# Kernel tuning notes

Hardware: AMD Instinct MI355X
Metric: run time of the kernel (lower is better)

The kernel has to match this reference:

```python
import jax, jax.numpy as jnp
import numpy as np

EPS = 1e-10


def setup_inputs() -> dict:
    key = jax.random.key(0)
    k1, k2, k3 = jax.random.split(key, 3)
    B, T, N = 32, 512, 128
    transition = jax.random.uniform(k1, (N, N), dtype=jnp.float32)
    log_emission = jax.random.normal(k2, (B, T, N), dtype=jnp.float32)
    prior = jax.random.uniform(k3, (N,), dtype=jnp.float32)
    return {"transition": transition, "log_emission": log_emission, "prior": prior}


def reference(transition, log_emission, prior):
    B, T, N = log_emission.shape
    # clamp + row-normalize transition (matches torch: clamp, clamp/sum(dim=1))
    trans = jnp.clip(transition, EPS)
    trans = jnp.clip(trans, EPS) / jnp.sum(trans, axis=1, keepdims=True)
    log_trans_T = jnp.log(trans).T  # (N, N): [next, prev]

    pr = jnp.clip(prior, EPS)
    pr = pr / jnp.sum(pr)
    log_prior = jnp.log(pr)

    # initial trellis row
    log0 = log_prior[None, :] + log_emission[:, 0]  # (B, N)
    em_rest = jnp.transpose(log_emission[:, 1:], (1, 0, 2))  # (T-1, B, N)

    def fwd_step(prev_log, em_t):
        # scores[b, next, prev] = prev_log[b, prev] + log_trans_T[next, prev]
        scores = prev_log[:, None, :] + log_trans_T[None, :, :]  # (B, N, N)
        m = jnp.max(scores, axis=-1, keepdims=True)
        e = jnp.exp(scores - m)
        Z = jnp.sum(e, axis=-1, keepdims=True)
        soft_max = jnp.squeeze(jnp.log(Z) + m, -1)  # logsumexp, (B, N)
        new_log = em_t + soft_max
        bp = e / Z  # soft backpointers, (B, N, N)
        return new_log, bp

    last_log, bps = jax.lax.scan(fwd_step, log0, em_rest)  # bps: (T-1, B, N, N)

    final_probs = jax.nn.softmax(last_log, axis=1)  # (B, N)

    def bwd_step(p_next, bp_t):
        # soft_path[t] = soft_path[t+1] @ bp[t]
        p = jnp.einsum("bn,bnm->bm", p_next, bp_t)
        return p, p

    _, path_prefix = jax.lax.scan(bwd_step, final_probs, bps, reverse=True)  # (T-1, B, N)

    soft_path = jnp.concatenate([path_prefix, final_probs[None]], axis=0)  # (T, B, N)
    return jnp.transpose(soft_path, (1, 0, 2))  # (B, T, N)
```

## Files before the change

### kernel.cpp

```cpp
#include <hip/hip_runtime.h>
#include <math.h>


#define TT 512
#define BB 32
#define NN 128
#define EPSC 1e-10f
#define TINY 1e-33f

typedef float v2f __attribute__((ext_vector_type(2)));

#define BAR() asm volatile("s_waitcnt lgkmcnt(0)\n\ts_barrier" ::: "memory")

__device__ __forceinline__ float rcp_fast(float x) {
  return __builtin_amdgcn_rcpf(x);
}

__device__ __forceinline__ float qswap1(float x) {
  return __int_as_float(__builtin_amdgcn_mov_dpp(__float_as_int(x), 0xB1, 0xF, 0xF, true));
}
__device__ __forceinline__ float qswap2(float x) {
  return __int_as_float(__builtin_amdgcn_mov_dpp(__float_as_int(x), 0x4E, 0xF, 0xF, true));
}

__device__ __forceinline__ float dotpk16(const v2f* av, const v2f tm[16]) {
  v2f a0 = av[0] * tm[0];
  v2f a1 = av[1] * tm[1];
  v2f a2 = av[2] * tm[2];
  v2f a3 = av[3] * tm[3];
  #pragma unroll
  for (int j = 4; j < 16; j += 4) {
    a0 = __builtin_elementwise_fma(av[j+0], tm[j+0], a0);
    a1 = __builtin_elementwise_fma(av[j+1], tm[j+1], a1);
    a2 = __builtin_elementwise_fma(av[j+2], tm[j+2], a2);
    a3 = __builtin_elementwise_fma(av[j+3], tm[j+3], a3);
  }
  v2f s = (a0 + a1) + (a2 + a3);
  return s.x + s.y;
}

__global__ __launch_bounds__(256, 1)
void soft_viterbi_kernel(const float* __restrict__ trans,
                         const float* __restrict__ emis,
                         const float* __restrict__ prior,
                         float* __restrict__ out) {
  const int b    = blockIdx.x;
  const int tid  = threadIdx.x;
  const int w    = tid >> 6;
  const int lane = tid & 63;
  const int k    = lane & 3;
  const int pid  = lane >> 2;
  const int n0   = 32 * w + 2 * pid;

  __shared__ __align__(16) float ubuf[2][NN];
  __shared__ __align__(16) float sarr[TT];
  __shared__ __align__(16) float red[NN];

  const float* emB = emis + (size_t)b * TT * NN;
  float* outb      = out  + (size_t)b * TT * NN;

  float2 pr2 = *(const float2*)(prior + n0);
  float2 em0 = *(const float2*)(emB + n0);
  float2 e1  = *(const float2*)(emB + 1 * NN + n0);
  float2 e2  = *(const float2*)(emB + 2 * NN + n0);
  float2 e3  = *(const float2*)(emB + 3 * NN + n0);
  float2 e4  = *(const float2*)(emB + 4 * NN + n0);
  float2 e5  = *(const float2*)(emB + 5 * NN + n0);
  pr2.x = fmaxf(pr2.x, EPSC); pr2.y = fmaxf(pr2.y, EPSC);

  if (tid < NN) {
    const float4* row = (const float4*)(trans + tid * NN);
    float s = 0.f;
    #pragma unroll 8
    for (int j = 0; j < NN / 4; ++j) {
      float4 v = row[j];
      s += fmaxf(v.x, EPSC) + fmaxf(v.y, EPSC) + fmaxf(v.z, EPSC) + fmaxf(v.w, EPSC);
    }
    red[tid] = s;
  }
  __syncthreads();

  v2f tf2[2][16];
  #pragma unroll
  for (int i = 0; i < 8; ++i) {
    #pragma unroll
    for (int c = 0; c < 4; ++c) {
      const int p = 4 * (k + 4 * i) + c;
      const float2 tv = *(const float2*)(trans + p * NN + n0);
      const float rp = red[p];
      tf2[0][2*i + (c >> 1)][c & 1] = fmaxf(tv.x, EPSC) / rp;
      tf2[1][2*i + (c >> 1)][c & 1] = fmaxf(tv.y, EPSC) / rp;
    }
  }
  v2f tb2[2][16];
  #pragma unroll
  for (int s = 0; s < 2; ++s) {
    const float inv = 1.0f / red[n0 + s];
    const float4* rr = (const float4*)(trans + (n0 + s) * NN);
    #pragma unroll
    for (int i = 0; i < 8; ++i) {
      const float4 tv = rr[k + 4 * i];
      tb2[s][2*i+0][0] = fmaxf(tv.x, EPSC) * inv;
      tb2[s][2*i+0][1] = fmaxf(tv.y, EPSC) * inv;
      tb2[s][2*i+1][0] = fmaxf(tv.z, EPSC) * inv;
      tb2[s][2*i+1][1] = fmaxf(tv.w, EPSC) * inv;
    }
  }

  float vv = (k == 0) ? (pr2.x + pr2.y) : 0.f;
  #pragma unroll
  for (int m = 1; m < 64; m <<= 1) vv += __shfl_xor(vv, m, 64);
  __syncthreads();
  if (lane == 0) red[w] = vv;
  __syncthreads();
  const float psum = (red[0] + red[1]) + (red[2] + red[3]);

  float an0 = (pr2.x / psum) * __expf(em0.x);
  float an1 = (pr2.y / psum) * __expf(em0.y);
  if (k == 0) {
    float2 a2v = make_float2(an0, an1);
    *(float2*)&ubuf[0][n0] = a2v;
    *(float2*)(outb + n0) = a2v;
  }
  float dc0 = __expf(e1.x), dc1 = __expf(e1.y);
  float2 rg0 = e4, rg1 = e5, rg2 = e2, rg3 = e3;
  BAR();

  auto fstep = [&](const float* rb, float* wb, int t, float2& slot) {
    const float r0 = rb[0];
    const float4* rb4 = (const float4*)rb;
    float4 a4[8];
    #pragma unroll
    for (int i = 0; i < 8; ++i) a4[i] = rb4[k + 4 * i];
    const v2f* av = (const v2f*)a4;
    float z0 = dotpk16(av, tf2[0]);
    float z1 = dotpk16(av, tf2[1]);
    z0 += qswap1(z0); z0 += qswap2(z0);
    z1 += qswap1(z1); z1 += qswap2(z1);
    const float rinv = rcp_fast(r0);
    an0 = (dc0 * rinv) * z0;
    an1 = (dc1 * rinv) * z1;
    dc0 = __expf(slot.x); dc1 = __expf(slot.y);
    const int tpre = (t + 5 < TT) ? (t + 5) : (TT - 1);
    const float* erow = emB + (size_t)tpre * NN;
    slot = *(const float2*)(erow + n0);
    if (k == 0) {
      float2 a2v = make_float2(an0, an1);
      *(float2*)(wb + n0) = a2v;
      if (t < TT - 1) {
        float* orow = outb + (size_t)t * NN;
        *(float2*)(orow + n0) = a2v;
      }
    }
    if (tid == 0) sarr[t - 1] = rinv;
    BAR();
  };

  fstep(ubuf[0], ubuf[1], 1, rg2);
  fstep(ubuf[1], ubuf[0], 2, rg3);
  fstep(ubuf[0], ubuf[1], 3, rg0);
  for (int t = 4; t < TT; t += 4) {
    fstep(ubuf[1], ubuf[0], t + 0, rg1);
    fstep(ubuf[0], ubuf[1], t + 1, rg2);
    fstep(ubuf[1], ubuf[0], t + 2, rg3);
    fstep(ubuf[0], ubuf[1], t + 3, rg0);
  }
  const float dl0 = dc0, dl1 = dc1;

  float v2 = (k == 0) ? (an0 + an1) : 0.f;
  #pragma unroll
  for (int m = 1; m < 64; m <<= 1) v2 += __shfl_xor(v2, m, 64);
  if (lane == 0) red[w] = v2;
  __syncthreads();
  const float total = (red[0] + red[1]) + (red[2] + red[3]);
  const float itot = 1.0f / total;
  float pc0 = an0 * itot, pc1 = an1 * itot;
  if (k == 0) *(float2*)(outb + (size_t)(TT - 1) * NN + n0) = make_float2(pc0, pc1);

  asm volatile("s_waitcnt vmcnt(0)" ::: "memory");

  float2 eb2 = *(const float2*)(emB  + (size_t)510 * NN + n0);
  float2 eb1 = *(const float2*)(emB  + (size_t)509 * NN + n0);
  float2 eb0 = *(const float2*)(emB  + (size_t)508 * NN + n0);
  float2 eb3 = *(const float2*)(emB  + (size_t)507 * NN + n0);
  float2 ac2 = *(const float2*)(outb + (size_t)510 * NN + n0);
  float2 ac1 = *(const float2*)(outb + (size_t)509 * NN + n0);
  float2 ac0 = *(const float2*)(outb + (size_t)508 * NN + n0);
  float2 ac3 = *(const float2*)(outb + (size_t)507 * NN + n0);
  const float sl = sarr[TT - 2];
  float g0 = dl0 * sl * rcp_fast(fmaxf(an0, TINY));
  float g1 = dl1 * sl * rcp_fast(fmaxf(an1, TINY));

  auto bstep = [&](float* xb, int t, float2& em_s, float2& ec_s) {
    if (k == 0) *(float2*)(xb + n0) = make_float2(pc0 * g0, pc1 * g1);
    const float sr = sarr[(t > 0) ? (t - 1) : 0];
    const float at0 = ec_s.x, at1 = ec_s.y;
    const float gn0 = __expf(em_s.x) * sr * rcp_fast(fmaxf(at0, TINY));
    const float gn1 = __expf(em_s.y) * sr * rcp_fast(fmaxf(at1, TINY));
    const int tp4 = (t >= 4) ? (t - 4) : 0;
    const float* erow = emB  + (size_t)tp4 * NN;
    const float* arow = outb + (size_t)tp4 * NN;
    em_s = *(const float2*)(erow + n0);
    ec_s = *(const float2*)(arow + n0);
    BAR();
    const float4* qb4 = (const float4*)xb;
    float4 a4[8];
    #pragma unroll
    for (int i = 0; i < 8; ++i) a4[i] = qb4[k + 4 * i];
    const v2f* av = (const v2f*)a4;
    float z0 = dotpk16(av, tb2[0]);
    float z1 = dotpk16(av, tb2[1]);
    z0 += qswap1(z0); z0 += qswap2(z0);
    z1 += qswap1(z1); z1 += qswap2(z1);
    pc0 = at0 * z0;
    pc1 = at1 * z1;
    if (k == 0) {
      float* orow = outb + (size_t)t * NN;
      *(float2*)(orow + n0) = make_float2(pc0, pc1);
    }
    g0 = gn0; g1 = gn1;
  };

  bstep(ubuf[0], 510, eb2, ac2);
  bstep(ubuf[1], 509, eb1, ac1);
  bstep(ubuf[0], 508, eb0, ac0);
  for (int t = 507; t >= 3; t -= 4) {
    bstep(ubuf[1], t - 0, eb3, ac3);
    bstep(ubuf[0], t - 1, eb2, ac2);
    bstep(ubuf[1], t - 2, eb1, ac1);
    bstep(ubuf[0], t - 3, eb0, ac0);
  }
}

extern "C" void kernel_launch(void* const* d_in, const int* in_sizes, int n_in,
                              void* d_out, int out_size, void* d_ws, size_t ws_size,
                              hipStream_t stream) {
  (void)in_sizes; (void)n_in; (void)d_ws; (void)ws_size; (void)out_size;
  const float* trans = (const float*)d_in[0];
  const float* emis  = (const float*)d_in[1];
  const float* prior = (const float*)d_in[2];
  float* out = (float*)d_out;
  soft_viterbi_kernel<<<dim3(BB), dim3(256), 0, stream>>>(trans, emis, prior, out);
}
```

Baseline: 399.4 us.

## Pack two batch sequences per 512-thread workgroup sharing barriers

Each workgroup now processes two batch elements using two 256-thread groups, with per-group LDS buffers, scale arrays and reduction slots, and launches half as many blocks. The intent is to interleave two independent serial recurrences on one CU so that one hides the other's latency. In exchange, every step's barrier now synchronises eight waves across both sequences, only half as many CUs are used, and launch_bounds(512,2) shrinks the per-thread register budget. That budget is tight for the large transition-matrix register arrays and may cause spilling.

```diff
diff --git a/kernel.cpp b/kernel.cpp
--- a/kernel.cpp
+++ b/kernel.cpp
@@ -15,7 +15,6 @@
 __device__ __forceinline__ float rcp_fast(float x) {
   return __builtin_amdgcn_rcpf(x);
 }
-
 __device__ __forceinline__ float qswap1(float x) {
   return __int_as_float(__builtin_amdgcn_mov_dpp(__float_as_int(x), 0xB1, 0xF, 0xF, true));
 }
@@ -39,22 +38,25 @@
   return s.x + s.y;
 }
 
-__global__ __launch_bounds__(256, 1)
+__global__ __launch_bounds__(512, 2)
 void soft_viterbi_kernel(const float* __restrict__ trans,
                          const float* __restrict__ emis,
                          const float* __restrict__ prior,
                          float* __restrict__ out) {
-  const int b    = blockIdx.x;
   const int tid  = threadIdx.x;
-  const int w    = tid >> 6;
+  const int GR   = tid >> 8;
+  const int t8   = tid & 255;
+  const int w    = t8 >> 6;
   const int lane = tid & 63;
   const int k    = lane & 3;
   const int pid  = lane >> 2;
   const int n0   = 32 * w + 2 * pid;
-
-  __shared__ __align__(16) float ubuf[2][NN];
-  __shared__ __align__(16) float sarr[TT];
+  const int b    = 2 * blockIdx.x + GR;
+
+  __shared__ __align__(16) float ubuf[2][2][NN];
+  __shared__ __align__(16) float sarr[2][TT];
   __shared__ __align__(16) float red[NN];
+  __shared__ float rsc[2][4];
 
   const float* emB = emis + (size_t)b * TT * NN;
   float* outb      = out  + (size_t)b * TT * NN;
@@ -110,16 +112,15 @@
   float vv = (k == 0) ? (pr2.x + pr2.y) : 0.f;
   #pragma unroll
   for (int m = 1; m < 64; m <<= 1) vv += __shfl_xor(vv, m, 64);
+  if (lane == 0) rsc[GR][w] = vv;
   __syncthreads();
-  if (lane == 0) red[w] = vv;
-  __syncthreads();
-  const float psum = (red[0] + red[1]) + (red[2] + red[3]);
+  const float psum = (rsc[GR][0] + rsc[GR][1]) + (rsc[GR][2] + rsc[GR][3]);
 
   float an0 = (pr2.x / psum) * __expf(em0.x);
   float an1 = (pr2.y / psum) * __expf(em0.y);
   if (k == 0) {
     float2 a2v = make_float2(an0, an1);
-    *(float2*)&ubuf[0][n0] = a2v;
+    *(float2*)&ubuf[GR][0][n0] = a2v;
     *(float2*)(outb + n0) = a2v;
   }
   float dc0 = __expf(e1.x), dc1 = __expf(e1.y);
@@ -152,27 +153,27 @@
         *(float2*)(orow + n0) = a2v;
       }
     }
-    if (tid == 0) sarr[t - 1] = rinv;
+    if (t8 == 0) sarr[GR][t - 1] = rinv;
     BAR();
   };
 
-  fstep(ubuf[0], ubuf[1], 1, rg2);
-  fstep(ubuf[1], ubuf[0], 2, rg3);
-  fstep(ubuf[0], ubuf[1], 3, rg0);
+  fstep(ubuf[GR][0], ubuf[GR][1], 1, rg2);
+  fstep(ubuf[GR][1], ubuf[GR][0], 2, rg3);
+  fstep(ubuf[GR][0], ubuf[GR][1], 3, rg0);
   for (int t = 4; t < TT; t += 4) {
-    fstep(ubuf[1], ubuf[0], t + 0, rg1);
-    fstep(ubuf[0], ubuf[1], t + 1, rg2);
-    fstep(ubuf[1], ubuf[0], t + 2, rg3);
-    fstep(ubuf[0], ubuf[1], t + 3, rg0);
+    fstep(ubuf[GR][1], ubuf[GR][0], t + 0, rg1);
+    fstep(ubuf[GR][0], ubuf[GR][1], t + 1, rg2);
+    fstep(ubuf[GR][1], ubuf[GR][0], t + 2, rg3);
+    fstep(ubuf[GR][0], ubuf[GR][1], t + 3, rg0);
   }
   const float dl0 = dc0, dl1 = dc1;
 
   float v2 = (k == 0) ? (an0 + an1) : 0.f;
   #pragma unroll
   for (int m = 1; m < 64; m <<= 1) v2 += __shfl_xor(v2, m, 64);
-  if (lane == 0) red[w] = v2;
+  if (lane == 0) rsc[GR][w] = v2;
   __syncthreads();
-  const float total = (red[0] + red[1]) + (red[2] + red[3]);
+  const float total = (rsc[GR][0] + rsc[GR][1]) + (rsc[GR][2] + rsc[GR][3]);
   const float itot = 1.0f / total;
   float pc0 = an0 * itot, pc1 = an1 * itot;
   if (k == 0) *(float2*)(outb + (size_t)(TT - 1) * NN + n0) = make_float2(pc0, pc1);
@@ -187,13 +188,13 @@
   float2 ac1 = *(const float2*)(outb + (size_t)509 * NN + n0);
   float2 ac0 = *(const float2*)(outb + (size_t)508 * NN + n0);
   float2 ac3 = *(const float2*)(outb + (size_t)507 * NN + n0);
-  const float sl = sarr[TT - 2];
+  const float sl = sarr[GR][TT - 2];
   float g0 = dl0 * sl * rcp_fast(fmaxf(an0, TINY));
   float g1 = dl1 * sl * rcp_fast(fmaxf(an1, TINY));
 
   auto bstep = [&](float* xb, int t, float2& em_s, float2& ec_s) {
     if (k == 0) *(float2*)(xb + n0) = make_float2(pc0 * g0, pc1 * g1);
-    const float sr = sarr[(t > 0) ? (t - 1) : 0];
+    const float sr = sarr[GR][(t > 0) ? (t - 1) : 0];
     const float at0 = ec_s.x, at1 = ec_s.y;
     const float gn0 = __expf(em_s.x) * sr * rcp_fast(fmaxf(at0, TINY));
     const float gn1 = __expf(em_s.y) * sr * rcp_fast(fmaxf(at1, TINY));
@@ -221,14 +222,14 @@
     g0 = gn0; g1 = gn1;
   };
 
-  bstep(ubuf[0], 510, eb2, ac2);
-  bstep(ubuf[1], 509, eb1, ac1);
-  bstep(ubuf[0], 508, eb0, ac0);
+  bstep(ubuf[GR][0], 510, eb2, ac2);
+  bstep(ubuf[GR][1], 509, eb1, ac1);
+  bstep(ubuf[GR][0], 508, eb0, ac0);
   for (int t = 507; t >= 3; t -= 4) {
-    bstep(ubuf[1], t - 0, eb3, ac3);
-    bstep(ubuf[0], t - 1, eb2, ac2);
-    bstep(ubuf[1], t - 2, eb1, ac1);
-    bstep(ubuf[0], t - 3, eb0, ac0);
+    bstep(ubuf[GR][1], t - 0, eb3, ac3);
+    bstep(ubuf[GR][0], t - 1, eb2, ac2);
+    bstep(ubuf[GR][1], t - 2, eb1, ac1);
+    bstep(ubuf[GR][0], t - 3, eb0, ac0);
   }
 }
 
@@ -240,5 +241,5 @@
   const float* emis  = (const float*)d_in[1];
   const float* prior = (const float*)d_in[2];
   float* out = (float*)d_out;
-  soft_viterbi_kernel<<<dim3(BB), dim3(256), 0, stream>>>(trans, emis, prior, out);
-}
+  soft_viterbi_kernel<<<dim3(BB / 2), dim3(512), 0, stream>>>(trans, emis, prior, out);
+}
```

Measured after the change: 505.3 us. 26.5% more time.

## Process two batch sequences per block to interleave independent recurrences

Applied to the files above, without the earlier changes.

Each block now handles two batch items instead of one, halving the grid to 16 blocks. The forward and backward steps for both sequences are interleaved, so independent dot products, DPP reductions and loads can hide each other's latency and each barrier is shared by two recurrences. The cost is roughly twice the per-step work and LDS traffic per block, and more register pressure, while only half as many CUs are used.

```diff
diff --git a/kernel.cpp b/kernel.cpp
--- a/kernel.cpp
+++ b/kernel.cpp
@@ -15,7 +15,6 @@
 __device__ __forceinline__ float rcp_fast(float x) {
   return __builtin_amdgcn_rcpf(x);
 }
-
 __device__ __forceinline__ float qswap1(float x) {
   return __int_as_float(__builtin_amdgcn_mov_dpp(__float_as_int(x), 0xB1, 0xF, 0xF, true));
 }
@@ -44,28 +43,38 @@
                          const float* __restrict__ emis,
                          const float* __restrict__ prior,
                          float* __restrict__ out) {
-  const int b    = blockIdx.x;
   const int tid  = threadIdx.x;
   const int w    = tid >> 6;
   const int lane = tid & 63;
   const int k    = lane & 3;
   const int pid  = lane >> 2;
   const int n0   = 32 * w + 2 * pid;
-
-  __shared__ __align__(16) float ubuf[2][NN];
-  __shared__ __align__(16) float sarr[TT];
+  const int bA   = 2 * blockIdx.x;
+  const int bB   = bA + 1;
+
+  __shared__ __align__(16) float ubuf[2][2][NN];
+  __shared__ __align__(16) float sarr[2][TT];
   __shared__ __align__(16) float red[NN];
-
-  const float* emB = emis + (size_t)b * TT * NN;
-  float* outb      = out  + (size_t)b * TT * NN;
+  __shared__ float rsc[2][4];
+
+  const float* emA = emis + (size_t)bA * TT * NN;
+  const float* emBp = emis + (size_t)bB * TT * NN;
+  float* outA = out + (size_t)bA * TT * NN;
+  float* outB = out + (size_t)bB * TT * NN;
 
   float2 pr2 = *(const float2*)(prior + n0);
-  float2 em0 = *(const float2*)(emB + n0);
-  float2 e1  = *(const float2*)(emB + 1 * NN + n0);
-  float2 e2  = *(const float2*)(emB + 2 * NN + n0);
-  float2 e3  = *(const float2*)(emB + 3 * NN + n0);
-  float2 e4  = *(const float2*)(emB + 4 * NN + n0);
-  float2 e5  = *(const float2*)(emB + 5 * NN + n0);
+  float2 em0A = *(const float2*)(emA + n0);
+  float2 em0B = *(const float2*)(emBp + n0);
+  float2 e1A = *(const float2*)(emA + 1 * NN + n0);
+  float2 e1B = *(const float2*)(emBp + 1 * NN + n0);
+  float2 e2A = *(const float2*)(emA + 2 * NN + n0);
+  float2 e2B = *(const float2*)(emBp + 2 * NN + n0);
+  float2 e3A = *(const float2*)(emA + 3 * NN + n0);
+  float2 e3B = *(const float2*)(emBp + 3 * NN + n0);
+  float2 e4A = *(const float2*)(emA + 4 * NN + n0);
+  float2 e4B = *(const float2*)(emBp + 4 * NN + n0);
+  float2 e5A = *(const float2*)(emA + 5 * NN + n0);
+  float2 e5B = *(const float2*)(emBp + 5 * NN + n0);
   pr2.x = fmaxf(pr2.x, EPSC); pr2.y = fmaxf(pr2.y, EPSC);
 
   if (tid < NN) {
@@ -111,124 +120,173 @@
   #pragma unroll
   for (int m = 1; m < 64; m <<= 1) vv += __shfl_xor(vv, m, 64);
   __syncthreads();
-  if (lane == 0) red[w] = vv;
+  if (lane == 0) rsc[0][w] = vv;
   __syncthreads();
-  const float psum = (red[0] + red[1]) + (red[2] + red[3]);
-
-  float an0 = (pr2.x / psum) * __expf(em0.x);
-  float an1 = (pr2.y / psum) * __expf(em0.y);
+  const float psum = (rsc[0][0] + rsc[0][1]) + (rsc[0][2] + rsc[0][3]);
+  const float ip0 = pr2.x / psum, ip1 = pr2.y / psum;
+
+  float anA0 = ip0 * __expf(em0A.x), anA1 = ip1 * __expf(em0A.y);
+  float anB0 = ip0 * __expf(em0B.x), anB1 = ip1 * __expf(em0B.y);
   if (k == 0) {
-    float2 a2v = make_float2(an0, an1);
-    *(float2*)&ubuf[0][n0] = a2v;
-    *(float2*)(outb + n0) = a2v;
-  }
-  float dc0 = __expf(e1.x), dc1 = __expf(e1.y);
-  float2 rg0 = e4, rg1 = e5, rg2 = e2, rg3 = e3;
+    *(float2*)&ubuf[0][0][n0] = make_float2(anA0, anA1);
+    *(float2*)&ubuf[1][0][n0] = make_float2(anB0, anB1);
+    *(float2*)(outA + n0) = make_float2(anA0, anA1);
+    *(float2*)(outB + n0) = make_float2(anB0, anB1);
+  }
+  float dcA0 = __expf(e1A.x), dcA1 = __expf(e1A.y);
+  float dcB0 = __expf(e1B.x), dcB1 = __expf(e1B.y);
+  float2 rgA0 = e4A, rgA1 = e5A, rgA2 = e2A, rgA3 = e3A;
+  float2 rgB0 = e4B, rgB1 = e5B, rgB2 = e2B, rgB3 = e3B;
   BAR();
 
-  auto fstep = [&](const float* rb, float* wb, int t, float2& slot) {
-    const float r0 = rb[0];
-    const float4* rb4 = (const float4*)rb;
-    float4 a4[8];
+  auto fstep = [&](int pp, int t, float2& slotA, float2& slotB) {
+    const float* rbA = ubuf[0][pp];
+    const float* rbB = ubuf[1][pp];
+    float* wbA = ubuf[0][pp ^ 1];
+    float* wbB = ubuf[1][pp ^ 1];
+    const float r0A = rbA[0];
+    const float r0B = rbB[0];
+    const float4* rb4A = (const float4*)rbA;
+    const float4* rb4B = (const float4*)rbB;
+    float4 a4A[8], a4B[8];
     #pragma unroll
-    for (int i = 0; i < 8; ++i) a4[i] = rb4[k + 4 * i];
-    const v2f* av = (const v2f*)a4;
-    float z0 = dotpk16(av, tf2[0]);
-    float z1 = dotpk16(av, tf2[1]);
-    z0 += qswap1(z0); z0 += qswap2(z0);
-    z1 += qswap1(z1); z1 += qswap2(z1);
-    const float rinv = rcp_fast(r0);
-    an0 = (dc0 * rinv) * z0;
-    an1 = (dc1 * rinv) * z1;
-    dc0 = __expf(slot.x); dc1 = __expf(slot.y);
+    for (int i = 0; i < 8; ++i) { a4A[i] = rb4A[k + 4 * i]; a4B[i] = rb4B[k + 4 * i]; }
+    const v2f* avA = (const v2f*)a4A;
+    const v2f* avB = (const v2f*)a4B;
+    float zA0 = dotpk16(avA, tf2[0]);
+    float zB0 = dotpk16(avB, tf2[0]);
+    float zA1 = dotpk16(avA, tf2[1]);
+    float zB1 = dotpk16(avB, tf2[1]);
+    zA0 += qswap1(zA0); zB0 += qswap1(zB0);
+    zA1 += qswap1(zA1); zB1 += qswap1(zB1);
+    zA0 += qswap2(zA0); zB0 += qswap2(zB0);
+    zA1 += qswap2(zA1); zB1 += qswap2(zB1);
+    const float rinvA = rcp_fast(r0A);
+    const float rinvB = rcp_fast(r0B);
+    anA0 = (dcA0 * rinvA) * zA0;  anA1 = (dcA1 * rinvA) * zA1;
+    anB0 = (dcB0 * rinvB) * zB0;  anB1 = (dcB1 * rinvB) * zB1;
+    dcA0 = __expf(slotA.x); dcA1 = __expf(slotA.y);
+    dcB0 = __expf(slotB.x); dcB1 = __expf(slotB.y);
     const int tpre = (t + 5 < TT) ? (t + 5) : (TT - 1);
-    const float* erow = emB + (size_t)tpre * NN;
-    slot = *(const float2*)(erow + n0);
+    slotA = *(const float2*)(emA  + (size_t)tpre * NN + n0);
+    slotB = *(const float2*)(emBp + (size_t)tpre * NN + n0);
     if (k == 0) {
-      float2 a2v = make_float2(an0, an1);
-      *(float2*)(wb + n0) = a2v;
+      *(float2*)(wbA + n0) = make_float2(anA0, anA1);
+      *(float2*)(wbB + n0) = make_float2(anB0, anB1);
       if (t < TT - 1) {
-        float* orow = outb + (size_t)t * NN;
-        *(float2*)(orow + n0) = a2v;
+        *(float2*)(outA + (size_t)t * NN + n0) = make_float2(anA0, anA1);
+        *(float2*)(outB + (size_t)t * NN + n0) = make_float2(anB0, anB1);
       }
     }
-    if (tid == 0) sarr[t - 1] = rinv;
+    if (tid == 0) { sarr[0][t - 1] = rinvA; sarr[1][t - 1] = rinvB; }
     BAR();
   };
 
-  fstep(ubuf[0], ubuf[1], 1, rg2);
-  fstep(ubuf[1], ubuf[0], 2, rg3);
-  fstep(ubuf[0], ubuf[1], 3, rg0);
+  fstep(0, 1, rgA2, rgB2);
+  fstep(1, 2, rgA3, rgB3);
+  fstep(0, 3, rgA0, rgB0);
   for (int t = 4; t < TT; t += 4) {
-    fstep(ubuf[1], ubuf[0], t + 0, rg1);
-    fstep(ubuf[0], ubuf[1], t + 1, rg2);
-    fstep(ubuf[1], ubuf[0], t + 2, rg3);
-    fstep(ubuf[0], ubuf[1], t + 3, rg0);
-  }
-  const float dl0 = dc0, dl1 = dc1;
-
-  float v2 = (k == 0) ? (an0 + an1) : 0.f;
-  #pragma unroll
-  for (int m = 1; m < 64; m <<= 1) v2 += __shfl_xor(v2, m, 64);
-  if (lane == 0) red[w] = v2;
+    fstep(1, t + 0, rgA1, rgB1);
+    fstep(0, t + 1, rgA2, rgB2);
+    fstep(1, t + 2, rgA3, rgB3);
+    fstep(0, t + 3, rgA0, rgB0);
+  }
+  const float dlA0 = dcA0, dlA1 = dcA1;
+  const float dlB0 = dcB0, dlB1 = dcB1;
+
+  float vA = (k == 0) ? (anA0 + anA1) : 0.f;
+  float vB = (k == 0) ? (anB0 + anB1) : 0.f;
+  #pragma unroll
+  for (int m = 1; m < 64; m <<= 1) { vA += __shfl_xor(vA, m, 64); vB += __shfl_xor(vB, m, 64); }
+  if (lane == 0) { rsc[0][w] = vA; rsc[1][w] = vB; }
   __syncthreads();
-  const float total = (red[0] + red[1]) + (red[2] + red[3]);
-  const float itot = 1.0f / total;
-  float pc0 = an0 * itot, pc1 = an1 * itot;
-  if (k == 0) *(float2*)(outb + (size_t)(TT - 1) * NN + n0) = make_float2(pc0, pc1);
+  const float itotA = 1.0f / ((rsc[0][0] + rsc[0][1]) + (rsc[0][2] + rsc[0][3]));
+  const float itotB = 1.0f / ((rsc[1][0] + rsc[1][1]) + (rsc[1][2] + rsc[1][3]));
+  float pcA0 = anA0 * itotA, pcA1 = anA1 * itotA;
+  float pcB0 = anB0 * itotB, pcB1 = anB1 * itotB;
+  if (k == 0) {
+    *(float2*)(outA + (size_t)(TT - 1) * NN + n0) = make_float2(pcA0, pcA1);
+    *(float2*)(outB + (size_t)(TT - 1) * NN + n0) = make_float2(pcB0, pcB1);
+  }
 
   asm volatile("s_waitcnt vmcnt(0)" ::: "memory");
 
-  float2 eb2 = *(const float2*)(emB  + (size_t)510 * NN + n0);
-  float2 eb1 = *(const float2*)(emB  + (size_t)509 * NN + n0);
-  float2 eb0 = *(const float2*)(emB  + (size_t)508 * NN + n0);
-  float2 eb3 = *(const float2*)(emB  + (size_t)507 * NN + n0);
-  float2 ac2 = *(const float2*)(outb + (size_t)510 * NN + n0);
-  float2 ac1 = *(const float2*)(outb + (size_t)509 * NN + n0);
-  float2 ac0 = *(const float2*)(outb + (size_t)508 * NN + n0);
-  float2 ac3 = *(const float2*)(outb + (size_t)507 * NN + n0);
-  const float sl = sarr[TT - 2];
-  float g0 = dl0 * sl * rcp_fast(fmaxf(an0, TINY));
-  float g1 = dl1 * sl * rcp_fast(fmaxf(an1, TINY));
-
-  auto bstep = [&](float* xb, int t, float2& em_s, float2& ec_s) {
-    if (k == 0) *(float2*)(xb + n0) = make_float2(pc0 * g0, pc1 * g1);
-    const float sr = sarr[(t > 0) ? (t - 1) : 0];
-    const float at0 = ec_s.x, at1 = ec_s.y;
-    const float gn0 = __expf(em_s.x) * sr * rcp_fast(fmaxf(at0, TINY));
-    const float gn1 = __expf(em_s.y) * sr * rcp_fast(fmaxf(at1, TINY));
+  float2 ebA2 = *(const float2*)(emA  + (size_t)510 * NN + n0);
+  float2 ebB2 = *(const float2*)(emBp + (size_t)510 * NN + n0);
+  float2 ebA1 = *(const float2*)(emA  + (size_t)509 * NN + n0);
+  float2 ebB1 = *(const float2*)(emBp + (size_t)509 * NN + n0);
+  float2 ebA0 = *(const float2*)(emA  + (size_t)508 * NN + n0);
+  float2 ebB0 = *(const float2*)(emBp + (size_t)508 * NN + n0);
+  float2 ebA3 = *(const float2*)(emA  + (size_t)507 * NN + n0);
+  float2 ebB3 = *(const float2*)(emBp + (size_t)507 * NN + n0);
+  float2 acA2 = *(const float2*)(outA + (size_t)510 * NN + n0);
+  float2 acB2 = *(const float2*)(outB + (size_t)510 * NN + n0);
+  float2 acA1 = *(const float2*)(outA + (size_t)509 * NN + n0);
+  float2 acB1 = *(const float2*)(outB + (size_t)509 * NN + n0);
+  float2 acA0 = *(const float2*)(outA + (size_t)508 * NN + n0);
+  float2 acB0 = *(const float2*)(outB + (size_t)508 * NN + n0);
+  float2 acA3 = *(const float2*)(outA + (size_t)507 * NN + n0);
+  float2 acB3 = *(const float2*)(outB + (size_t)507 * NN + n0);
+  const float slA = sarr[0][TT - 2];
+  const float slB = sarr[1][TT - 2];
+  float gA0 = dlA0 * slA * rcp_fast(fmaxf(anA0, TINY));
+  float gA1 = dlA1 * slA * rcp_fast(fmaxf(anA1, TINY));
+  float gB0 = dlB0 * slB * rcp_fast(fmaxf(anB0, TINY));
+  float gB1 = dlB1 * slB * rcp_fast(fmaxf(anB1, TINY));
+
+  auto bstep = [&](int pp, int t, float2& emsA, float2& ecsA, float2& emsB, float2& ecsB) {
+    float* xbA = ubuf[0][pp];
+    float* xbB = ubuf[1][pp];
+    if (k == 0) {
+      *(float2*)(xbA + n0) = make_float2(pcA0 * gA0, pcA1 * gA1);
+      *(float2*)(xbB + n0) = make_float2(pcB0 * gB0, pcB1 * gB1);
+    }
+    const float srA = sarr[0][(t > 0) ? (t - 1) : 0];
+    const float srB = sarr[1][(t > 0) ? (t - 1) : 0];
+    const float atA0 = ecsA.x, atA1 = ecsA.y;
+    const float atB0 = ecsB.x, atB1 = ecsB.y;
+    const float gnA0 = __expf(emsA.x) * srA * rcp_fast(fmaxf(atA0, TINY));
+    const float gnA1 = __expf(emsA.y) * srA * rcp_fast(fmaxf(atA1, TINY));
+    const float gnB0 = __expf(emsB.x) * srB * rcp_fast(fmaxf(atB0, TINY));
+    const float gnB1 = __expf(emsB.y) * srB * rcp_fast(fmaxf(atB1, TINY));
     const int tp4 = (t >= 4) ? (t - 4) : 0;
-    const float* erow = emB  + (size_t)tp4 * NN;
-    const float* arow = outb + (size_t)tp4 * NN;
-    em_s = *(const float2*)(erow + n0);
-    ec_s = *(const float2*)(arow + n0);
+    emsA = *(const float2*)(emA  + (size_t)tp4 * NN + n0);
+    emsB = *(const float2*)(emBp + (size_t)tp4 * NN + n0);
+    ecsA = *(const float2*)(outA + (size_t)tp4 * NN + n0);
+    ecsB = *(const float2*)(outB + (size_t)tp4 * NN + n0);
     BAR();
-    const float4* qb4 = (const float4*)xb;
-    float4 a4[8];
+    const float4* qb4A = (const float4*)xbA;
+    const float4* qb4B = (const float4*)xbB;
+    float4 a4A[8], a4B[8];
     #pragma unroll
-    for (int i = 0; i < 8; ++i) a4[i] = qb4[k + 4 * i];
-    const v2f* av = (const v2f*)a4;
-    float z0 = dotpk16(av, tb2[0]);
-    float z1 = dotpk16(av, tb2[1]);
-    z0 += qswap1(z0); z0 += qswap2(z0);
-    z1 += qswap1(z1); z1 += qswap2(z1);
-    pc0 = at0 * z0;
-    pc1 = at1 * z1;
+    for (int i = 0; i < 8; ++i) { a4A[i] = qb4A[k + 4 * i]; a4B[i] = qb4B[k + 4 * i]; }
+    const v2f* avA = (const v2f*)a4A;
+    const v2f* avB = (const v2f*)a4B;
+    float zA0 = dotpk16(avA, tb2[0]);
+    float zB0 = dotpk16(avB, tb2[0]);
+    float zA1 = dotpk16(avA, tb2[1]);
+    float zB1 = dotpk16(avB, tb2[1]);
+    zA0 += qswap1(zA0); zB0 += qswap1(zB0);
+    zA1 += qswap1(zA1); zB1 += qswap1(zB1);
+    zA0 += qswap2(zA0); zB0 += qswap2(zB0);
+    zA1 += qswap2(zA1); zB1 += qswap2(zB1);
+    pcA0 = atA0 * zA0;  pcA1 = atA1 * zA1;
+    pcB0 = atB0 * zB0;  pcB1 = atB1 * zB1;
     if (k == 0) {
-      float* orow = outb + (size_t)t * NN;
-      *(float2*)(orow + n0) = make_float2(pc0, pc1);
-    }
-    g0 = gn0; g1 = gn1;
+      *(float2*)(outA + (size_t)t * NN + n0) = make_float2(pcA0, pcA1);
+      *(float2*)(outB + (size_t)t * NN + n0) = make_float2(pcB0, pcB1);
+    }
+    gA0 = gnA0; gA1 = gnA1; gB0 = gnB0; gB1 = gnB1;
   };
 
-  bstep(ubuf[0], 510, eb2, ac2);
-  bstep(ubuf[1], 509, eb1, ac1);
-  bstep(ubuf[0], 508, eb0, ac0);
+  bstep(0, 510, ebA2, acA2, ebB2, acB2);
+  bstep(1, 509, ebA1, acA1, ebB1, acB1);
+  bstep(0, 508, ebA0, acA0, ebB0, acB0);
   for (int t = 507; t >= 3; t -= 4) {
-    bstep(ubuf[1], t - 0, eb3, ac3);
-    bstep(ubuf[0], t - 1, eb2, ac2);
-    bstep(ubuf[1], t - 2, eb1, ac1);
-    bstep(ubuf[0], t - 3, eb0, ac0);
+    bstep(1, t - 0, ebA3, acA3, ebB3, acB3);
+    bstep(0, t - 1, ebA2, acA2, ebB2, acB2);
+    bstep(1, t - 2, ebA1, acA1, ebB1, acB1);
+    bstep(0, t - 3, ebA0, acA0, ebB0, acB0);
   }
 }
 
@@ -240,5 +298,5 @@
   const float* emis  = (const float*)d_in[1];
   const float* prior = (const float*)d_in[2];
   float* out = (float*)d_out;
-  soft_viterbi_kernel<<<dim3(BB), dim3(256), 0, stream>>>(trans, emis, prior, out);
-}
+  soft_viterbi_kernel<<<dim3(BB / 2), dim3(256), 0, stream>>>(trans, emis, prior, out);
+}
```

Measured after the change: 583.9 us. 1.46x slower.
